# Performance work log

Hardware: AMD Instinct MI355X
Metric: run time of the kernel (lower is better)

## Reference

```python
import jax, jax.numpy as jnp
import numpy as np

N, K, H, W = 2048, 8, 128, 128
G = 50              # glimpse size (50x50 from tem_rnn input 50*50)
ENC = 100           # glimpse encoder output (relation_rnn input arithmetic)
HID = 256
D_REL = ENC + (3 + 50) * 2 + HID          # 462
D_TEM = G * G + (3 + 50) * 2 + HID        # 2862


def _lin(k, out_d, in_d, scale=0.02):
    k1, k2 = jax.random.split(k)
    return (jax.random.normal(k1, (out_d, in_d), jnp.float32) * scale,
            jax.random.normal(k2, (out_d,), jnp.float32) * scale)


def _lstm_params(k, in_d, hid):
    k1, k2, k3, k4 = jax.random.split(k, 4)
    s = 0.02
    return (jax.random.normal(k1, (4 * hid, in_d), jnp.float32) * s,
            jax.random.normal(k2, (4 * hid, hid), jnp.float32) * s,
            jax.random.normal(k3, (4 * hid,), jnp.float32) * s,
            jax.random.normal(k4, (4 * hid,), jnp.float32) * s)


def lstm_cell(x, h, c, Wih, Whh, bih, bhh):
    g = x @ Wih.T + h @ Whh.T + (bih + bhh)
    i, f, gg, o = jnp.split(g, 4, axis=-1)
    i, f, o = jax.nn.sigmoid(i), jax.nn.sigmoid(f), jax.nn.sigmoid(o)
    c2 = f * c + i * jnp.tanh(gg)
    return o * jnp.tanh(c2), c2


def _bilinear_one(im, py, px):
    # im [H,W]; py,px [G,G] pixel coords; zeros padding like torch grid_sample
    x0 = jnp.floor(px); y0 = jnp.floor(py)
    wx1 = px - x0; wy1 = py - y0
    x0i = x0.astype(jnp.int32); y0i = y0.astype(jnp.int32)

    def gather(yi, xi):
        valid = (yi >= 0) & (yi < H) & (xi >= 0) & (xi < W)
        v = im[jnp.clip(yi, 0, H - 1), jnp.clip(xi, 0, W - 1)]
        return jnp.where(valid, v, 0.0)

    return ((1 - wy1) * (1 - wx1) * gather(y0i, x0i)
            + (1 - wy1) * wx1 * gather(y0i, x0i + 1)
            + wy1 * (1 - wx1) * gather(y0i + 1, x0i)
            + wy1 * wx1 * gather(y0i + 1, x0i + 1))


def stn_glimpse(z_where, img):
    # z_where [n,3] = (scale, tx, ty); theta = [[s,0,tx],[0,s,ty]] (attentive_stn_encode)
    s, tx, ty = z_where[:, 0], z_where[:, 1], z_where[:, 2]
    lin = jnp.linspace(-1.0, 1.0, G)
    gy, gx = jnp.meshgrid(lin, lin, indexing='ij')           # [G,G]
    px = (s[:, None, None] * gx + tx[:, None, None] + 1.0) * 0.5 * (W - 1)
    py = (s[:, None, None] * gy + ty[:, None, None] + 1.0) * 0.5 * (H - 1)
    out = jax.vmap(_bilinear_one)(img, py, px)               # [n,G,G]
    return out.reshape(out.shape[0], G * G)


def setup_inputs() -> dict:
    key = jax.random.key(0)
    ks = jax.random.split(key, 16)
    inp = {
        'img': jax.random.uniform(ks[0], (N, H, W), jnp.float32),
        'z_what_last': jax.random.normal(ks[1], (N, K, 50), jnp.float32),
        'z_where_last': jax.random.normal(ks[2], (N, K, 3), jnp.float32) * 0.3,
        'z_pres_last': jnp.ones((N, K, 1), jnp.float32),
        'hidden_last': jax.random.normal(ks[3], (N, K, HID), jnp.float32),
    }
    inp['W_loca'], inp['b_loca'] = _lin(ks[4], 3, HID)
    inp['Wg'], inp['bg'] = _lin(ks[5], ENC, G * G)
    (inp['Wih_rel'], inp['Whh_rel'], inp['bih_rel'], inp['bhh_rel']) = _lstm_params(ks[6], D_REL, HID)
    (inp['Wih_tem'], inp['Whh_tem'], inp['bih_tem'], inp['bhh_tem']) = _lstm_params(ks[7], D_TEM, HID)
    inp['Wm_wh'], inp['bm_wh'] = _lin(ks[8], 3, HID + 3)
    inp['Ws_wh'], inp['bs_wh'] = _lin(ks[9], 3, HID + 3)
    inp['Wm_wt'], inp['bm_wt'] = _lin(ks[10], 50, 50 + HID + HID)
    inp['Ws_wt'], inp['bs_wt'] = _lin(ks[11], 50, 50 + HID + HID)
    inp['Wm_pr'], inp['bm_pr'] = _lin(ks[12], 1, 50 + 3 + HID + HID)
    inp['Ws_pr'], inp['bs_pr'] = _lin(ks[13], 1, 50 + 3 + HID + HID)
    return inp


def reference(img, z_what_last, z_where_last, z_pres_last, hidden_last,
              W_loca, b_loca, Wg, bg,
              Wih_rel, Whh_rel, bih_rel, bhh_rel,
              Wih_tem, Whh_tem, bih_tem, bhh_tem,
              Wm_wh, bm_wh, Ws_wh, bs_wh,
              Wm_wt, bm_wt, Ws_wt, bs_wt,
              Wm_pr, bm_pr, Ws_pr, bs_pr):
    n = img.shape[0]

    def step(carry, xs):
        h_r, c_r, pzw, pzwhat = carry
        zwl, zwhatl, zpl, hl = xs   # [n,3],[n,50],[n,1],[n,256]
        # prop_loca: relu(linear(hidden)) + z_where_last
        zwb = jax.nn.relu(hl @ W_loca.T + b_loca) + zwl
        # STN glimpse + encode (bias pass)
        enc = jax.nn.relu(stn_glimpse(zwb, img) @ Wg.T + bg)        # [n,100]
        rin = jnp.concatenate([enc, zwl, pzw, zwhatl, pzwhat, hl], -1)  # [n,462]
        h_r2, c_r2 = lstm_cell(rin, h_r, c_r, Wih_rel, Whh_rel, bih_rel, bhh_rel)
        # z_where: latent predictor mean (eval mode)
        zw = jnp.concatenate([zwl, h_r2], -1) @ Wm_wh.T + bm_wh      # [n,3]
        # second STN glimpse with sampled where
        g2 = stn_glimpse(zw, img)                                    # [n,2500]
        tin = jnp.concatenate([g2, zw, pzw, zwhatl, pzwhat, hl], -1) # [n,2862]
        h_t, c_t = lstm_cell(tin, h_r2, c_r2, Wih_tem, Whh_tem, bih_tem, bhh_tem)
        # z_what mean
        zwhat = jnp.concatenate([zwhatl, h_r2, h_t], -1) @ Wm_wt.T + bm_wt  # [n,50]
        # z_pres: deterministic expectation of Bernoulli(mean*std) * previous pres
        zp_cal = jnp.concatenate([zwhat, zw, h_r2, h_t], -1)
        p = jax.nn.sigmoid(zp_cal @ Wm_pr.T + bm_pr) * jax.nn.sigmoid(zp_cal @ Ws_pr.T + bs_pr)
        zp = p * zpl                                                 # [n,1]
        return (h_r2, c_r2, zw, zwhat), (zwhat, zw, zp, h_t)

    carry0 = (jnp.zeros((n, HID), img.dtype), jnp.zeros((n, HID), img.dtype),
              jnp.zeros((n, 3), img.dtype), jnp.zeros((n, 50), img.dtype))
    xs = (jnp.swapaxes(z_where_last, 0, 1), jnp.swapaxes(z_what_last, 0, 1),
          jnp.swapaxes(z_pres_last, 0, 1), jnp.swapaxes(hidden_last, 0, 1))
    _, (zwhat_s, zw_s, zp_s, ht_s) = jax.lax.scan(step, carry0, xs)
    z_what = jnp.swapaxes(zwhat_s, 0, 1)   # [n,K,50]
    z_where = jnp.swapaxes(zw_s, 0, 1)     # [n,K,3]
    z_pres = jnp.swapaxes(zp_s, 0, 1)      # [n,K,1]
    h_temp = jnp.swapaxes(ht_s, 0, 1)      # [n,K,256]
    return z_what, z_where, z_pres, h_temp
```

## Files before the change

### kernel.cpp

```cpp
#include <hip/hip_runtime.h>
#include <hip/hip_bf16.h>
#include <math.h>

typedef __attribute__((ext_vector_type(8))) short bf16x8;
typedef __attribute__((ext_vector_type(4))) float f32x4;
using bf16 = __hip_bfloat16;

constexpr int NN   = 2048;
constexpr int KO   = 8;
constexpr int IH   = 128, IW = 128;
constexpr int GS   = 50;
constexpr int HIDD = 256;
constexpr int RIN_LD = 768;
constexpr int TIN_LD = 3136;
constexpr int G1_LD  = 2560;
constexpr int GSTR   = NN*1024;

__device__ __forceinline__ float sigm(float x) { return 1.f/(1.f+expf(-x)); }

template<int OUT_BF16, int RELU>
__global__ __launch_bounds__(256, 4) void mfma_gemm(
    const bf16* __restrict__ A, int lda, int Ktot,
    const bf16* __restrict__ Wt, int ldw, int M,
    const float* __restrict__ b1, const float* __restrict__ b2,
    void* __restrict__ Cout, int ldc, int nxb, int Kseg, int sstride)
{
    __shared__ __align__(16) bf16 As[2*4096];
    __shared__ __align__(16) bf16 Bs[2*4096];
    const int b    = blockIdx.x;
    const int xcd  = b & 7;
    const int t    = b >> 3;
    const int n0   = (xcd + 8*(t / nxb))*64;
    const int m0   = (t % nxb)*64;
    const int tid  = threadIdx.x;
    const int w    = tid>>6, lane = tid&63;
    const int wy   = w>>1, wx = w&1;
    const int q    = lane>>4, fr = lane&15;

    const int kbeg = blockIdx.y * Kseg;
    const int kend = min(Ktot, kbeg + Kseg);
    const int nk   = (kend - kbeg) >> 6;

    const int r0   = tid>>3;
    const int csrc = ((tid&7)*8) ^ ((r0&7)<<3);
    const bf16* pa = A + (size_t)(n0 + r0)*lda + kbeg + csrc;
    int wmr0 = m0 + r0;       if (wmr0 > M-1) wmr0 = M-1;
    int wmr1 = m0 + r0 + 32;  if (wmr1 > M-1) wmr1 = M-1;
    const bf16* pb  = Wt + (size_t)wmr0*ldw + kbeg + csrc;
    const bf16* pb1 = Wt + (size_t)wmr1*ldw + kbeg + csrc;

    f32x4 acc[2][2] = {};

    auto stage = [&](int buf, int koff) {
        bf16* la = As + buf*4096 + w*512;
        bf16* lb = Bs + buf*4096 + w*512;
        __builtin_amdgcn_global_load_lds(
            (const __attribute__((address_space(1))) void*)(pa + koff),
            (__attribute__((address_space(3))) void*)la, 16, 0, 0);
        __builtin_amdgcn_global_load_lds(
            (const __attribute__((address_space(1))) void*)(pa + koff + 32*(size_t)lda),
            (__attribute__((address_space(3))) void*)(la + 2048), 16, 0, 0);
        __builtin_amdgcn_global_load_lds(
            (const __attribute__((address_space(1))) void*)(pb + koff),
            (__attribute__((address_space(3))) void*)lb, 16, 0, 0);
        __builtin_amdgcn_global_load_lds(
            (const __attribute__((address_space(1))) void*)(pb1 + koff),
            (__attribute__((address_space(3))) void*)(lb + 2048), 16, 0, 0);
    };

    stage(0, 0);
    __syncthreads();
    int cur = 0;
    for (int kt = 0; kt < nk; ++kt) {
        if (kt + 1 < nk) stage(cur ^ 1, (kt + 1) << 6);
        const bf16* Ab = As + cur*4096;
        const bf16* Bb = Bs + cur*4096;
        bf16x8 av[2][2], bv[2][2];
        #pragma unroll
        for (int i=0;i<2;i++) {
            int r = wy*32 + i*16 + fr;
            int sw = (r&7)<<3, base = r*64;
            av[i][0] = *(const bf16x8*)(Ab + base + ((q*8) ^ sw));
            av[i][1] = *(const bf16x8*)(Ab + base + ((32 + q*8) ^ sw));
        }
        #pragma unroll
        for (int j=0;j<2;j++) {
            int r = wx*32 + j*16 + fr;
            int sw = (r&7)<<3, base = r*64;
            bv[j][0] = *(const bf16x8*)(Bb + base + ((q*8) ^ sw));
            bv[j][1] = *(const bf16x8*)(Bb + base + ((32 + q*8) ^ sw));
        }
        #pragma unroll
        for (int h=0;h<2;h++)
            #pragma unroll
            for (int i=0;i<2;i++)
                #pragma unroll
                for (int j=0;j<2;j++)
                    acc[i][j] = __builtin_amdgcn_mfma_f32_16x16x32_bf16(av[i][h], bv[j][h], acc[i][j], 0, 0, 0);
        __syncthreads();
        cur ^= 1;
    }

    #pragma unroll
    for (int j=0;j<2;j++) {
        int col = m0 + wx*32 + j*16 + fr;
        if (col < M) {
            float bias = 0.f;
            if (blockIdx.y == 0) {
                if (b1) bias += b1[col];
                if (b2) bias += b2[col];
            }
            #pragma unroll
            for (int i=0;i<2;i++) {
                #pragma unroll
                for (int reg=0;reg<4;reg++) {
                    float v = acc[i][j][reg] + bias;
                    if (RELU) v = fmaxf(v, 0.f);
                    size_t idx = (size_t)(n0 + wy*32 + i*16 + q*4 + reg)*ldc + col;
                    if (OUT_BF16) ((bf16*)Cout)[idx] = __float2bfloat16(v);
                    else          ((float*)Cout)[(size_t)blockIdx.y*sstride + idx] = v;
                }
            }
        }
    }
}

template<int JT>
__global__ __launch_bounds__(256, 2) void gemm128(
    const bf16* __restrict__ A, int lda, int Ktot,
    const bf16* __restrict__ Wt, int ldw,
    const float* __restrict__ b1, const float* __restrict__ b2,
    float* __restrict__ Cout, int ldc, int nxb, int Kseg, int sstride)
{
    constexpr int BMC = JT*32;
    __shared__ __align__(16) bf16 As[128*64];
    __shared__ __align__(16) bf16 Bs[BMC*64];
    const int b    = blockIdx.x;
    const int xcd  = b & 7;
    const int t    = b >> 3;
    const int n0   = (xcd + 8*(t / nxb))*128;
    const int m0   = (t % nxb)*BMC;
    const int tid  = threadIdx.x;
    const int w    = tid>>6, lane = tid&63;
    const int wy   = w>>1, wx = w&1;
    const int q    = lane>>4, fr = lane&15;

    const int kbeg = blockIdx.y * Kseg;
    const int kend = min(Ktot, kbeg + Kseg);
    const int nk   = (kend - kbeg) >> 6;

    const int r0 = tid>>3;
    const int c0 = (tid&7)*8;

    f32x4 acc[4][JT] = {};

    for (int kt = 0; kt < nk; ++kt) {
        const int koff = kbeg + (kt<<6);
        __syncthreads();
        #pragma unroll
        for (int p=0;p<4;p++) {
            int row = p*32 + r0;
            int csrc = c0 ^ ((row&7)<<3);
            __builtin_amdgcn_global_load_lds(
                (const __attribute__((address_space(1))) void*)(A + (size_t)(n0+row)*lda + koff + csrc),
                (__attribute__((address_space(3))) void*)(As + p*2048 + w*512), 16, 0, 0);
        }
        #pragma unroll
        for (int p=0;p<JT;p++) {
            int row = p*32 + r0;
            int csrc = c0 ^ ((row&7)<<3);
            __builtin_amdgcn_global_load_lds(
                (const __attribute__((address_space(1))) void*)(Wt + (size_t)(m0+row)*ldw + koff + csrc),
                (__attribute__((address_space(3))) void*)(Bs + p*2048 + w*512), 16, 0, 0);
        }
        __syncthreads();
        #pragma unroll
        for (int h=0;h<2;h++) {
            bf16x8 av[4], bv[JT];
            #pragma unroll
            for (int i=0;i<4;i++) {
                int r = wy*64 + i*16 + fr;
                av[i] = *(const bf16x8*)(As + r*64 + ((h*32 + q*8) ^ ((r&7)<<3)));
            }
            #pragma unroll
            for (int j=0;j<JT;j++) {
                int r = wx*(JT*16) + j*16 + fr;
                bv[j] = *(const bf16x8*)(Bs + r*64 + ((h*32 + q*8) ^ ((r&7)<<3)));
            }
            #pragma unroll
            for (int i=0;i<4;i++)
                #pragma unroll
                for (int j=0;j<JT;j++)
                    acc[i][j] = __builtin_amdgcn_mfma_f32_16x16x32_bf16(av[i], bv[j], acc[i][j], 0, 0, 0);
        }
    }

    float* Cb = Cout + (size_t)blockIdx.y*sstride;
    #pragma unroll
    for (int j=0;j<JT;j++) {
        int col = m0 + wx*(JT*16) + j*16 + fr;
        float bias = 0.f;
        if (blockIdx.y == 0) {
            if (b1) bias += b1[col];
            if (b2) bias += b2[col];
        }
        #pragma unroll
        for (int i=0;i<4;i++)
            #pragma unroll
            for (int reg=0;reg<4;reg++)
                Cb[(size_t)(n0 + wy*64 + i*16 + q*4 + reg)*ldc + col] = acc[i][j][reg] + bias;
    }
}

__global__ __launch_bounds__(512) void glimpse_all(const float* __restrict__ img,
                                                   const float* __restrict__ zwb,
                                                   bf16* __restrict__ dst, int ldd,
                                                   bf16* __restrict__ rin,
                                                   const float* __restrict__ z_where_last,
                                                   const float* __restrict__ z_what_last,
                                                   const float* __restrict__ hidden_last,
                                                   int cbase, int CH) {
    __shared__ float im_s[IH*IW];
    __shared__ float xw0[KO*50], xw1[KO*50];
    __shared__ int   xi0[KO*50], xi1[KO*50];
    __shared__ float yw0[KO*50], yw1[KO*50];
    __shared__ int   yr0[KO*50], yr1[KO*50];
    const int n = blockIdx.x;
    const float* im = img + (size_t)n*IH*IW;
    {
        const float4* s4 = (const float4*)im;
        float4* d4 = (float4*)im_s;
        for (int t = threadIdx.x; t < IH*IW/4; t += 512) d4[t] = s4[t];
    }
    const float GXS = 2.0f/49.0f;
    for (int t = threadIdx.x; t < CH*100; t += 512) {
        int sl = t / 100, r = t - sl*100;
        const float* zr = zwb + (size_t)(sl*NN + n)*3;
        float s = zr[0];
        if (r < 50) {
            float txp = zr[1] + 1.0f;
            float gx = fmaf((float)r, GXS, -1.0f);
            float px = fmaf(s, gx, txp)*63.5f;
            float x0f = floorf(px); float fa = px - x0f; int x0 = (int)x0f;
            xw0[sl*50+r] = ((unsigned)x0     < 128u) ? (1.f - fa) : 0.f;
            xw1[sl*50+r] = ((unsigned)(x0+1) < 128u) ? fa         : 0.f;
            xi0[sl*50+r] = min(max(x0,  0),127);
            xi1[sl*50+r] = min(max(x0+1,0),127);
        } else {
            int i = r - 50;
            float typ = zr[2] + 1.0f;
            float gy = fmaf((float)i, GXS, -1.0f);
            float py = fmaf(s, gy, typ)*63.5f;
            float y0f = floorf(py); float fy = py - y0f; int y0 = (int)y0f;
            yw0[sl*50+i] = ((unsigned)y0     < 128u) ? (1.f - fy) : 0.f;
            yw1[sl*50+i] = ((unsigned)(y0+1) < 128u) ? fy         : 0.f;
            yr0[sl*50+i] = min(max(y0,  0),127)*IW;
            yr1[sl*50+i] = min(max(y0+1,0),127)*IW;
        }
    }
    __syncthreads();

    const int tot = CH*1250;
    for (int p = threadIdx.x; p < tot; p += 512) {
        int sl = p / 1250, p2 = p - sl*1250;
        int i = p2 / 25, j = (p2 - i*25)*2;
        const float* r0 = im_s + yr0[sl*50+i];
        const float* r1 = im_s + yr1[sl*50+i];
        float wy0 = yw0[sl*50+i], wy1 = yw1[sl*50+i];
        int   a0 = xi0[sl*50+j],     a1 = xi1[sl*50+j];
        float wa0 = xw0[sl*50+j],    wa1 = xw1[sl*50+j];
        int   e0 = xi0[sl*50+j+1],   e1 = xi1[sl*50+j+1];
        float wb0 = xw0[sl*50+j+1],  wb1 = xw1[sl*50+j+1];
        float va = fmaf(wy1, fmaf(wa0, r1[a0], wa1*r1[a1]),
                   wy0 *     fmaf(wa0, r0[a0], wa1*r0[a1]));
        float vb = fmaf(wy1, fmaf(wb0, r1[e0], wb1*r1[e1]),
                   wy0 *     fmaf(wb0, r0[e0], wb1*r0[e1]));
        bf16 b0 = __float2bfloat16(va), b1 = __float2bfloat16(vb);
        unsigned short u0, u1;
        __builtin_memcpy(&u0, &b0, 2); __builtin_memcpy(&u1, &b1, 2);
        bf16* drow = dst + (size_t)(sl*NN + n)*ldd;
        *(unsigned int*)(drow + i*GS + j) = (unsigned)u0 | ((unsigned)u1 << 16);
    }

    const int tot2 = CH*309;
    for (int t = threadIdx.x; t < tot2; t += 512) {
        int sl = t / 309, c = t - sl*309;
        int k = cbase + sl;
        bf16* rrow = rin + (size_t)(sl*NN + n)*RIN_LD;
        float v; int col;
        if (c < 3)       { col = 100 + c;      v = z_where_last[((size_t)n*KO + k)*3 + c]; }
        else if (c < 53) { col = 106 + (c-3);  v = z_what_last[((size_t)n*KO + k)*50 + (c-3)]; }
        else             { col = 206 + (c-53); v = hidden_last[((size_t)n*KO + k)*HIDD + (c-53)]; }
        rrow[col] = __float2bfloat16(v);
    }
}

__global__ __launch_bounds__(256) void rel_glimpse2(
    const float* __restrict__ gates, int nsplit,
    float* __restrict__ h_r, float* __restrict__ c_r,
    const float* __restrict__ z_where_last,
    const float* __restrict__ Wm_wh, const float* __restrict__ bm_wh,
    float* __restrict__ zw_cur, float* __restrict__ out_zwhere,
    bf16* __restrict__ rin_next, bf16* __restrict__ tin,
    const float* __restrict__ img,
    const float* __restrict__ zw_prev, const float* __restrict__ zwhat_prev,
    const float* __restrict__ z_what_last, const float* __restrict__ hidden_last, int k)
{
    __shared__ float hs[256];
    __shared__ float zws[3];
    __shared__ float xw0[50], xw1[50], yw0[50], yw1[50];
    __shared__ int   xi0[50], xi1[50], yr0[50], yr1[50];
    int n = blockIdx.x, j = threadIdx.x;
    float sI=0.f, sF=0.f, sG=0.f, sO=0.f;
    for (int p = 0; p < nsplit; ++p) {
        const float* g = gates + (size_t)p*GSTR + (size_t)n*1024;
        sI += g[j]; sF += g[256+j]; sG += g[512+j]; sO += g[768+j];
    }
    float ig = sigm(sI), fg = sigm(sF), gg = tanhf(sG), og = sigm(sO);
    int cidx = n*256 + j;
    float c2 = fg*c_r[cidx] + ig*gg;
    float hv = og*tanhf(c2);
    c_r[cidx] = c2;
    h_r[cidx] = hv;
    hs[j] = hv;
    bf16 hb = __float2bfloat16(hv);
    rin_next[(size_t)n*RIN_LD + 462 + j] = hb;
    bf16* trow = tin + (size_t)n*TIN_LD;
    trow[2862 + j] = hb;
    __syncthreads();
    int w = j >> 6, lane = j & 63;
    if (w < 3) {
        const float* wt = Wm_wh + w*259;
        float sa = 0.f;
        for (int i = lane; i < 256; i += 64) sa = fmaf(hs[i], wt[3+i], sa);
        #pragma unroll
        for (int off = 32; off; off >>= 1) sa += __shfl_down(sa, off);
        if (lane == 0) {
            const float* zwl = z_where_last + ((size_t)n*KO + k)*3;
            float acc = bm_wh[w] + sa;
            for (int i = 0; i < 3; i++) acc = fmaf(zwl[i], wt[i], acc);
            zws[w] = acc;
            zw_cur[n*3+w] = acc;
            out_zwhere[((size_t)n*KO + k)*3 + w] = acc;
            bf16 ab = __float2bfloat16(acc);
            rin_next[(size_t)n*RIN_LD + 103 + w] = ab;
            trow[2500 + w] = ab;
        }
    }
    __syncthreads();
    {
        const float GXS = 2.0f/49.0f;
        float s = zws[0];
        if (j < 50) {
            float txp = zws[1] + 1.0f;
            float gx = fmaf((float)j, GXS, -1.0f);
            float px = fmaf(s, gx, txp)*63.5f;
            float x0f = floorf(px); float fa = px - x0f; int x0 = (int)x0f;
            xw0[j] = ((unsigned)x0     < 128u) ? (1.f - fa) : 0.f;
            xw1[j] = ((unsigned)(x0+1) < 128u) ? fa         : 0.f;
            xi0[j] = min(max(x0,  0),127);
            xi1[j] = min(max(x0+1,0),127);
        } else if (j < 100) {
            int i = j - 50;
            float typ = zws[2] + 1.0f;
            float gy = fmaf((float)i, GXS, -1.0f);
            float py = fmaf(s, gy, typ)*63.5f;
            float y0f = floorf(py); float fy = py - y0f; int y0 = (int)y0f;
            yw0[i] = ((unsigned)y0     < 128u) ? (1.f - fy) : 0.f;
            yw1[i] = ((unsigned)(y0+1) < 128u) ? fy         : 0.f;
            yr0[i] = min(max(y0,  0),127)*IW;
            yr1[i] = min(max(y0+1,0),127)*IW;
        }
    }
    __syncthreads();
    const float* im = img + (size_t)n*IH*IW;
    for (int p2 = j; p2 < 1250; p2 += 256) {
        int i = p2 / 25, jj = (p2 - i*25)*2;
        const float* r0 = im + yr0[i];
        const float* r1 = im + yr1[i];
        float wy0 = yw0[i], wy1 = yw1[i];
        int   a0 = xi0[jj],    a1 = xi1[jj];
        float wa0 = xw0[jj],   wa1 = xw1[jj];
        int   e0 = xi0[jj+1],  e1 = xi1[jj+1];
        float wb0 = xw0[jj+1], wb1 = xw1[jj+1];
        float va = fmaf(wy1, fmaf(wa0, r1[a0], wa1*r1[a1]),
                   wy0 *     fmaf(wa0, r0[a0], wa1*r0[a1]));
        float vb = fmaf(wy1, fmaf(wb0, r1[e0], wb1*r1[e1]),
                   wy0 *     fmaf(wb0, r0[e0], wb1*r0[e1]));
        bf16 b0 = __float2bfloat16(va), b1 = __float2bfloat16(vb);
        unsigned short u0, u1;
        __builtin_memcpy(&u0, &b0, 2); __builtin_memcpy(&u1, &b1, 2);
        *(unsigned int*)(trow + i*GS + jj) = (unsigned)u0 | ((unsigned)u1 << 16);
    }
    for (int c = 3 + j; c < 362; c += 256) {
        float v;
        if      (c <   6) v = zw_prev[n*3 + c-3];
        else if (c <  56) v = z_what_last[((size_t)n*KO + k)*50 + c-6];
        else if (c < 106) v = zwhat_prev[n*50 + c-56];
        else              v = hidden_last[((size_t)n*KO + k)*HIDD + c-106];
        trow[2500 + c] = __float2bfloat16(v);
    }
}

__global__ void zero_f32(float* __restrict__ p, int n) {
    int i = blockIdx.x*blockDim.x + threadIdx.x;
    if (i < n) p[i] = 0.f;
}

__global__ void repack_w(const float* __restrict__ s1, int K1,
                         const float* __restrict__ s2, int K2,
                         bf16* __restrict__ dst, int ldd, int M) {
    int gid = blockIdx.x*blockDim.x + threadIdx.x;
    if (gid >= M*ldd) return;
    int m = gid / ldd, c = gid - m*ldd;
    float v = 0.f;
    if (c < K1)           v = s1[(size_t)m*K1 + c];
    else if (c < K1+K2)   v = s2[(size_t)m*K2 + (c-K1)];
    dst[gid] = __float2bfloat16(v);
}

__global__ void transpose_wmwt(const float* __restrict__ W, float* __restrict__ Wt) {
    int gid = blockIdx.x*blockDim.x + threadIdx.x;
    if (gid >= 576*64) return;
    int i = gid >> 6, m = gid & 63;
    Wt[gid] = (m < 50 && i < 562) ? W[(size_t)m*562 + i] : 0.f;
}

__global__ __launch_bounds__(256) void zwb_all_v2(const float* __restrict__ hidden_last,
                                                  const float* __restrict__ z_where_last,
                                                  const float* __restrict__ Wl, const float* __restrict__ bl,
                                                  float* __restrict__ zwb_all) {
    __shared__ float wls[768];
    for (int i = threadIdx.x; i < 768; i += 256) wls[i] = Wl[i];
    __syncthreads();
    int wv = threadIdx.x>>6, lane = threadIdx.x&63;
    int row = blockIdx.x*4 + wv;
    int s = row >> 11, n = row & (NN-1);
    const float* hl = hidden_last + ((size_t)n*KO + s)*HIDD;
    float4 h4 = *(const float4*)(hl + lane*4);
    float s0=0.f, s1=0.f, s2=0.f;
    #pragma unroll
    for (int r4=0;r4<4;r4++) {
        float hv = ((const float*)&h4)[r4];
        int i = lane*4 + r4;
        s0 = fmaf(hv, wls[i],     s0);
        s1 = fmaf(hv, wls[256+i], s1);
        s2 = fmaf(hv, wls[512+i], s2);
    }
    #pragma unroll
    for (int off=32; off; off>>=1) {
        s0 += __shfl_down(s0,off); s1 += __shfl_down(s1,off); s2 += __shfl_down(s2,off);
    }
    if (lane == 0) {
        const float* zwl = z_where_last + ((size_t)n*KO + s)*3;
        zwb_all[row*3+0] = fmaxf(s0+bl[0],0.f) + zwl[0];
        zwb_all[row*3+1] = fmaxf(s1+bl[1],0.f) + zwl[1];
        zwb_all[row*3+2] = fmaxf(s2+bl[2],0.f) + zwl[2];
    }
}

__global__ void zero_rin_carry(bf16* __restrict__ rin0) {
    int gid = blockIdx.x*blockDim.x + threadIdx.x;
    if (gid >= NN*309) return;
    int c = gid % 309, n = gid/309;
    int col = (c < 3) ? 103+c : ((c < 53) ? 156+(c-3) : 462+(c-53));
    rin0[(size_t)n*RIN_LD + col] = __float2bfloat16(0.f);
}

__global__ __launch_bounds__(256) void tem_fused(
    const float* __restrict__ gates, int nsplit,
    const float* __restrict__ c_r, const float* __restrict__ h_r,
    const float* __restrict__ z_what_last,
    const float* __restrict__ wt_t, const float* __restrict__ bm_wt,
    const float* __restrict__ Wm_pr, const float* __restrict__ bm_pr,
    const float* __restrict__ Ws_pr, const float* __restrict__ bs_pr,
    const float* __restrict__ zw_cur, const float* __restrict__ z_pres_last,
    float* __restrict__ zwhat_cur, float* __restrict__ out_zwhat,
    float* __restrict__ out_htemp, float* __restrict__ out_zpres,
    bf16* __restrict__ rin_next, int k)
{
    __shared__ float L[615];
    __shared__ float part[4][64];
    int n = blockIdx.x, j = threadIdx.x;
    float sI=0.f, sF=0.f, sG=0.f, sO=0.f;
    for (int p = 0; p < nsplit; ++p) {
        const float* g = gates + (size_t)p*GSTR + (size_t)n*1024;
        sI += g[j]; sF += g[256+j]; sG += g[512+j]; sO += g[768+j];
    }
    float ig = sigm(sI), fg = sigm(sF), gg = tanhf(sG), og = sigm(sO);
    float c2 = fg*c_r[n*256+j] + ig*gg;
    float hv = og*tanhf(c2);
    out_htemp[((size_t)n*KO + k)*HIDD + j] = hv;
    L[309+j] = hv;
    L[53+j]  = h_r[n*256+j];
    if (j < 50)      L[j]  = z_what_last[((size_t)n*KO + k)*50 + j];
    else if (j < 53) L[j]  = zw_cur[n*3 + (j-50)];
    __syncthreads();
    {
        int m = j & 63, grp = j >> 6;
        float sa = 0.f;
        for (int i = grp; i < 562; i += 4) {
            float v = (i < 50) ? L[i] : L[i+3];
            sa = fmaf(v, wt_t[i*64 + m], sa);
        }
        part[grp][m] = sa;
    }
    __syncthreads();
    if (j < 50) {
        float acc = part[0][j] + part[1][j] + part[2][j] + part[3][j] + bm_wt[j];
        zwhat_cur[n*50+j] = acc;
        out_zwhat[((size_t)n*KO + k)*50 + j] = acc;
        rin_next[(size_t)n*RIN_LD + 156 + j] = __float2bfloat16(acc);
        L[565+j] = acc;
    }
    __syncthreads();
    if (j < 64) {
        float s1 = 0.f, s2 = 0.f;
        for (int i = j; i < 565; i += 64) {
            float v = (i < 50) ? L[565+i] : L[i];
            s1 = fmaf(v, Wm_pr[i], s1);
            s2 = fmaf(v, Ws_pr[i], s2);
        }
        #pragma unroll
        for (int off = 32; off; off >>= 1) { s1 += __shfl_down(s1,off); s2 += __shfl_down(s2,off); }
        if (j == 0) {
            float p = sigm(s1 + bm_pr[0]) * sigm(s2 + bs_pr[0]);
            out_zpres[(size_t)n*KO + k] = p * z_pres_last[(size_t)n*KO + k];
        }
    }
}

extern "C" void kernel_launch(void* const* d_in, const int* in_sizes, int n_in,
                              void* d_out, int out_size, void* d_ws, size_t ws_size,
                              hipStream_t stream) {
    (void)in_sizes; (void)n_in; (void)out_size;
    const float* img          = (const float*)d_in[0];
    const float* z_what_last  = (const float*)d_in[1];
    const float* z_where_last = (const float*)d_in[2];
    const float* z_pres_last  = (const float*)d_in[3];
    const float* hidden_last  = (const float*)d_in[4];
    const float* W_loca = (const float*)d_in[5];
    const float* b_loca = (const float*)d_in[6];
    const float* Wg     = (const float*)d_in[7];
    const float* bg     = (const float*)d_in[8];
    const float* Wih_rel = (const float*)d_in[9];
    const float* Whh_rel = (const float*)d_in[10];
    const float* bih_rel = (const float*)d_in[11];
    const float* bhh_rel = (const float*)d_in[12];
    const float* Wih_tem = (const float*)d_in[13];
    const float* Whh_tem = (const float*)d_in[14];
    const float* bih_tem = (const float*)d_in[15];
    const float* bhh_tem = (const float*)d_in[16];
    const float* Wm_wh = (const float*)d_in[17];
    const float* bm_wh = (const float*)d_in[18];
    const float* Wm_wt = (const float*)d_in[21];
    const float* bm_wt = (const float*)d_in[22];
    const float* Wm_pr = (const float*)d_in[25];
    const float* bm_pr = (const float*)d_in[26];
    const float* Ws_pr = (const float*)d_in[27];
    const float* bs_pr = (const float*)d_in[28];

    char* base_p = (char*)d_ws;
    size_t off = 0;
    auto carve = [&](size_t bytes) -> char* {
        char* r = base_p + off;
        off += (bytes + 255) & ~(size_t)255;
        return r;
    };
    bf16*  tin      = (bf16*) carve((size_t)NN*TIN_LD*2);
    float* gates    = (float*)carve((size_t)4*NN*1024*4);
    bf16*  W_tem    = (bf16*) carve((size_t)1024*TIN_LD*2);
    bf16*  W_rel    = (bf16*) carve((size_t)1024*RIN_LD*2);
    bf16*  Wg_bf    = (bf16*) carve((size_t)100*G1_LD*2);
    float* wt_t     = (float*)carve((size_t)576*64*4);
    float* zwb_all  = (float*)carve((size_t)KO*NN*3*4);
    float* h_r      = (float*)carve((size_t)NN*HIDD*4);
    float* c_r      = (float*)carve((size_t)NN*HIDD*4);
    float* zw1      = (float*)carve((size_t)NN*3*4);
    float* zwhat1   = (float*)carve((size_t)NN*50*4);
    float* zw0      = (float*)carve((size_t)NN*3*4);
    float* zwhat0   = (float*)carve((size_t)NN*50*4);
    size_t fixed_bytes = off;

    int CH = 1;
    for (int cand : {8, 4, 2}) {
        size_t need = fixed_bytes
                    + (((size_t)cand*NN*G1_LD*2 + 255) & ~(size_t)255)
                    + (((size_t)cand*NN*RIN_LD*2 + 255) & ~(size_t)255);
        if (need <= ws_size) { CH = cand; break; }
    }
    bf16* g1 = nullptr; int g1ld;
    bf16* rin;
    if (CH > 1) {
        g1   = (bf16*)carve((size_t)CH*NN*G1_LD*2);
        rin  = (bf16*)carve((size_t)CH*NN*RIN_LD*2);
        g1ld = G1_LD;
    } else {
        rin  = (bf16*)carve((size_t)NN*RIN_LD*2);
        g1   = tin;
        g1ld = TIN_LD;
    }

    float* out        = (float*)d_out;
    float* out_zwhat  = out;
    float* out_zwhere = out + (size_t)NN*KO*50;
    float* out_zpres  = out_zwhere + (size_t)NN*KO*3;
    float* out_htemp  = out_zpres + (size_t)NN*KO;

    {
        int nz = NN*(HIDD + 3 + 50);
        zero_f32<<<(nz+255)/256, 256, 0, stream>>>(c_r, nz);
    }
    zero_rin_carry<<<(NN*309+255)/256, 256, 0, stream>>>(rin);
    repack_w<<<((1024*RIN_LD)+255)/256, 256, 0, stream>>>(Wih_rel, 462, Whh_rel, 256, W_rel, RIN_LD, 1024);
    repack_w<<<((1024*TIN_LD)+255)/256, 256, 0, stream>>>(Wih_tem, 2862, Whh_tem, 256, W_tem, TIN_LD, 1024);
    repack_w<<<((100*G1_LD)+255)/256, 256, 0, stream>>>(Wg, 2500, nullptr, 0, Wg_bf, G1_LD, 100);
    transpose_wmwt<<<(576*64+255)/256, 256, 0, stream>>>(Wm_wt, wt_t);
    zwb_all_v2<<<KO*NN/4, 256, 0, stream>>>(hidden_last, z_where_last, W_loca, b_loca, zwb_all);

    for (int cbase = 0; cbase < KO; cbase += CH) {
        glimpse_all<<<NN, 512, 0, stream>>>(img, zwb_all + (size_t)cbase*NN*3, g1, g1ld,
                                            rin, z_where_last, z_what_last, hidden_last, cbase, CH);
        mfma_gemm<1,1><<<dim3(2*CH*32,1), 256, 0, stream>>>(g1, g1ld, G1_LD, Wg_bf, G1_LD, 100,
                                                            bg, nullptr, rin, RIN_LD, 2, G1_LD, 0);

        for (int s = 0; s < CH; ++s) {
            int k = cbase + s;
            bf16* rin_k  = rin + (size_t)s*NN*RIN_LD;
            bf16* rin_nx = rin + (size_t)((s+1)%CH)*NN*RIN_LD;
            float* zw_cur     = (k & 1) ? zw1 : zw0;
            float* zw_prev    = (k & 1) ? zw0 : zw1;
            float* zwhat_cur  = (k & 1) ? zwhat1 : zwhat0;
            float* zwhat_prev = (k & 1) ? zwhat0 : zwhat1;

            gemm128<2><<<dim3(256,2), 256, 0, stream>>>(rin_k, RIN_LD, RIN_LD, W_rel, RIN_LD,
                                                        bih_rel, bhh_rel, gates, 1024, 16, 384, GSTR);
            rel_glimpse2<<<NN, 256, 0, stream>>>(gates, 2, h_r, c_r, z_where_last, Wm_wh, bm_wh,
                                                 zw_cur, out_zwhere, rin_nx, tin,
                                                 img, zw_prev, zwhat_prev, z_what_last, hidden_last, k);
            gemm128<4><<<dim3(128,4), 256, 0, stream>>>(tin, TIN_LD, TIN_LD, W_tem, TIN_LD,
                                                        bih_tem, bhh_tem, gates, 1024, 8, 832, GSTR);
            tem_fused<<<NN, 256, 0, stream>>>(gates, 4, c_r, h_r, z_what_last, wt_t, bm_wt, Wm_pr, bm_pr, Ws_pr, bs_pr,
                                              zw_cur, z_pres_last, zwhat_cur, out_zwhat, out_htemp, out_zpres, rin_nx, k);
        }
    }
}
```

Before: 1.126 ms.

## Fuse glimpse sampling with encoder GEMM and reshape temporal GEMM split

The glimpse kernel now samples straight from global memory, with no LDS copy of the image. It keeps the bf16 glimpse tile for all objects in LDS and runs the 100-output encoder matmul with MFMA inside the same block, writing ReLU outputs into the relation input. This removes the separate glimpse buffer, its global round trip and the extra GEMM launch. The temporal LSTM GEMM switches from a 4-way to a 2-way K split with narrower tiles, which halves the partial-sum gate storage that tem_fused has to read. Risks are uncoalesced global image gathers, and the in-block MFMA using only 7 waves with strided global weight loads.

```diff
diff --git a/kernel.cpp b/kernel.cpp
--- a/kernel.cpp
+++ b/kernel.cpp
@@ -13,117 +13,10 @@
 constexpr int HIDD = 256;
 constexpr int RIN_LD = 768;
 constexpr int TIN_LD = 3136;
-constexpr int G1_LD  = 2560;
+constexpr int WG_LD  = 2560;
 constexpr int GSTR   = NN*1024;
 
 __device__ __forceinline__ float sigm(float x) { return 1.f/(1.f+expf(-x)); }
-
-template<int OUT_BF16, int RELU>
-__global__ __launch_bounds__(256, 4) void mfma_gemm(
-    const bf16* __restrict__ A, int lda, int Ktot,
-    const bf16* __restrict__ Wt, int ldw, int M,
-    const float* __restrict__ b1, const float* __restrict__ b2,
-    void* __restrict__ Cout, int ldc, int nxb, int Kseg, int sstride)
-{
-    __shared__ __align__(16) bf16 As[2*4096];
-    __shared__ __align__(16) bf16 Bs[2*4096];
-    const int b    = blockIdx.x;
-    const int xcd  = b & 7;
-    const int t    = b >> 3;
-    const int n0   = (xcd + 8*(t / nxb))*64;
-    const int m0   = (t % nxb)*64;
-    const int tid  = threadIdx.x;
-    const int w    = tid>>6, lane = tid&63;
-    const int wy   = w>>1, wx = w&1;
-    const int q    = lane>>4, fr = lane&15;
-
-    const int kbeg = blockIdx.y * Kseg;
-    const int kend = min(Ktot, kbeg + Kseg);
-    const int nk   = (kend - kbeg) >> 6;
-
-    const int r0   = tid>>3;
-    const int csrc = ((tid&7)*8) ^ ((r0&7)<<3);
-    const bf16* pa = A + (size_t)(n0 + r0)*lda + kbeg + csrc;
-    int wmr0 = m0 + r0;       if (wmr0 > M-1) wmr0 = M-1;
-    int wmr1 = m0 + r0 + 32;  if (wmr1 > M-1) wmr1 = M-1;
-    const bf16* pb  = Wt + (size_t)wmr0*ldw + kbeg + csrc;
-    const bf16* pb1 = Wt + (size_t)wmr1*ldw + kbeg + csrc;
-
-    f32x4 acc[2][2] = {};
-
-    auto stage = [&](int buf, int koff) {
-        bf16* la = As + buf*4096 + w*512;
-        bf16* lb = Bs + buf*4096 + w*512;
-        __builtin_amdgcn_global_load_lds(
-            (const __attribute__((address_space(1))) void*)(pa + koff),
-            (__attribute__((address_space(3))) void*)la, 16, 0, 0);
-        __builtin_amdgcn_global_load_lds(
-            (const __attribute__((address_space(1))) void*)(pa + koff + 32*(size_t)lda),
-            (__attribute__((address_space(3))) void*)(la + 2048), 16, 0, 0);
-        __builtin_amdgcn_global_load_lds(
-            (const __attribute__((address_space(1))) void*)(pb + koff),
-            (__attribute__((address_space(3))) void*)lb, 16, 0, 0);
-        __builtin_amdgcn_global_load_lds(
-            (const __attribute__((address_space(1))) void*)(pb1 + koff),
-            (__attribute__((address_space(3))) void*)(lb + 2048), 16, 0, 0);
-    };
-
-    stage(0, 0);
-    __syncthreads();
-    int cur = 0;
-    for (int kt = 0; kt < nk; ++kt) {
-        if (kt + 1 < nk) stage(cur ^ 1, (kt + 1) << 6);
-        const bf16* Ab = As + cur*4096;
-        const bf16* Bb = Bs + cur*4096;
-        bf16x8 av[2][2], bv[2][2];
-        #pragma unroll
-        for (int i=0;i<2;i++) {
-            int r = wy*32 + i*16 + fr;
-            int sw = (r&7)<<3, base = r*64;
-            av[i][0] = *(const bf16x8*)(Ab + base + ((q*8) ^ sw));
-            av[i][1] = *(const bf16x8*)(Ab + base + ((32 + q*8) ^ sw));
-        }
-        #pragma unroll
-        for (int j=0;j<2;j++) {
-            int r = wx*32 + j*16 + fr;
-            int sw = (r&7)<<3, base = r*64;
-            bv[j][0] = *(const bf16x8*)(Bb + base + ((q*8) ^ sw));
-            bv[j][1] = *(const bf16x8*)(Bb + base + ((32 + q*8) ^ sw));
-        }
-        #pragma unroll
-        for (int h=0;h<2;h++)
-            #pragma unroll
-            for (int i=0;i<2;i++)
-                #pragma unroll
-                for (int j=0;j<2;j++)
-                    acc[i][j] = __builtin_amdgcn_mfma_f32_16x16x32_bf16(av[i][h], bv[j][h], acc[i][j], 0, 0, 0);
-        __syncthreads();
-        cur ^= 1;
-    }
-
-    #pragma unroll
-    for (int j=0;j<2;j++) {
-        int col = m0 + wx*32 + j*16 + fr;
-        if (col < M) {
-            float bias = 0.f;
-            if (blockIdx.y == 0) {
-                if (b1) bias += b1[col];
-                if (b2) bias += b2[col];
-            }
-            #pragma unroll
-            for (int i=0;i<2;i++) {
-                #pragma unroll
-                for (int reg=0;reg<4;reg++) {
-                    float v = acc[i][j][reg] + bias;
-                    if (RELU) v = fmaxf(v, 0.f);
-                    size_t idx = (size_t)(n0 + wy*32 + i*16 + q*4 + reg)*ldc + col;
-                    if (OUT_BF16) ((bf16*)Cout)[idx] = __float2bfloat16(v);
-                    else          ((float*)Cout)[(size_t)blockIdx.y*sstride + idx] = v;
-                }
-            }
-        }
-    }
-}
 
 template<int JT>
 __global__ __launch_bounds__(256, 2) void gemm128(
@@ -212,28 +105,25 @@
     }
 }
 
-__global__ __launch_bounds__(512) void glimpse_all(const float* __restrict__ img,
-                                                   const float* __restrict__ zwb,
-                                                   bf16* __restrict__ dst, int ldd,
-                                                   bf16* __restrict__ rin,
-                                                   const float* __restrict__ z_where_last,
-                                                   const float* __restrict__ z_what_last,
-                                                   const float* __restrict__ hidden_last,
-                                                   int cbase, int CH) {
-    __shared__ float im_s[IH*IW];
-    __shared__ float xw0[KO*50], xw1[KO*50];
-    __shared__ int   xi0[KO*50], xi1[KO*50];
-    __shared__ float yw0[KO*50], yw1[KO*50];
-    __shared__ int   yr0[KO*50], yr1[KO*50];
-    const int n = blockIdx.x;
-    const float* im = img + (size_t)n*IH*IW;
-    {
-        const float4* s4 = (const float4*)im;
-        float4* d4 = (float4*)im_s;
-        for (int t = threadIdx.x; t < IH*IW/4; t += 512) d4[t] = s4[t];
-    }
+__global__ __launch_bounds__(512) void glimpse_enc(
+    const float* __restrict__ img,
+    const float* __restrict__ zwb,
+    const bf16*  __restrict__ Wg_bf,
+    const float* __restrict__ bg,
+    bf16* __restrict__ rin,
+    const float* __restrict__ z_where_last,
+    const float* __restrict__ z_what_last,
+    const float* __restrict__ hidden_last,
+    int cbase, int CH)
+{
+    __shared__ float xw0[8*50], xw1[8*50], yw0[8*50], yw1[8*50];
+    __shared__ int   xi01[8*50], yro01[8*50];
+    __shared__ __align__(16) unsigned g_u[8*1264];
+    const int n   = blockIdx.x;
+    const int tid = threadIdx.x;
     const float GXS = 2.0f/49.0f;
-    for (int t = threadIdx.x; t < CH*100; t += 512) {
+
+    for (int t = tid; t < CH*100; t += 512) {
         int sl = t / 100, r = t - sl*100;
         const float* zr = zwb + (size_t)(sl*NN + n)*3;
         float s = zr[0];
@@ -244,8 +134,7 @@
             float x0f = floorf(px); float fa = px - x0f; int x0 = (int)x0f;
             xw0[sl*50+r] = ((unsigned)x0     < 128u) ? (1.f - fa) : 0.f;
             xw1[sl*50+r] = ((unsigned)(x0+1) < 128u) ? fa         : 0.f;
-            xi0[sl*50+r] = min(max(x0,  0),127);
-            xi1[sl*50+r] = min(max(x0+1,0),127);
+            xi01[sl*50+r] = min(max(x0,0),127) | (min(max(x0+1,0),127) << 16);
         } else {
             int i = r - 50;
             float typ = zr[2] + 1.0f;
@@ -254,23 +143,29 @@
             float y0f = floorf(py); float fy = py - y0f; int y0 = (int)y0f;
             yw0[sl*50+i] = ((unsigned)y0     < 128u) ? (1.f - fy) : 0.f;
             yw1[sl*50+i] = ((unsigned)(y0+1) < 128u) ? fy         : 0.f;
-            yr0[sl*50+i] = min(max(y0,  0),127)*IW;
-            yr1[sl*50+i] = min(max(y0+1,0),127)*IW;
-        }
-    }
-    __syncthreads();
-
+            yro01[sl*50+i] = (min(max(y0,0),127)*IW) | ((min(max(y0+1,0),127)*IW) << 16);
+        }
+    }
+    for (int t = tid; t < 8*14; t += 512) {
+        int sl = t / 14;
+        g_u[sl*1264 + 1250 + (t - sl*14)] = 0u;
+    }
+    __syncthreads();
+
+    const float* im = img + (size_t)n*IH*IW;
     const int tot = CH*1250;
-    for (int p = threadIdx.x; p < tot; p += 512) {
+    for (int p = tid; p < tot; p += 512) {
         int sl = p / 1250, p2 = p - sl*1250;
-        int i = p2 / 25, j = (p2 - i*25)*2;
-        const float* r0 = im_s + yr0[sl*50+i];
-        const float* r1 = im_s + yr1[sl*50+i];
+        int i = p2 / 25, jh = p2 - i*25;
+        int j = jh*2;
+        int yy = yro01[sl*50+i];
+        const float* r0 = im + (yy & 0xffff);
+        const float* r1 = im + (yy >> 16);
         float wy0 = yw0[sl*50+i], wy1 = yw1[sl*50+i];
-        int   a0 = xi0[sl*50+j],     a1 = xi1[sl*50+j];
-        float wa0 = xw0[sl*50+j],    wa1 = xw1[sl*50+j];
-        int   e0 = xi0[sl*50+j+1],   e1 = xi1[sl*50+j+1];
-        float wb0 = xw0[sl*50+j+1],  wb1 = xw1[sl*50+j+1];
+        int xa = xi01[sl*50+j];   int a0 = xa & 0xffff, a1 = xa >> 16;
+        float wa0 = xw0[sl*50+j], wa1 = xw1[sl*50+j];
+        int xb = xi01[sl*50+j+1]; int e0 = xb & 0xffff, e1 = xb >> 16;
+        float wb0 = xw0[sl*50+j+1], wb1 = xw1[sl*50+j+1];
         float va = fmaf(wy1, fmaf(wa0, r1[a0], wa1*r1[a1]),
                    wy0 *     fmaf(wa0, r0[a0], wa1*r0[a1]));
         float vb = fmaf(wy1, fmaf(wb0, r1[e0], wb1*r1[e1]),
@@ -278,12 +173,10 @@
         bf16 b0 = __float2bfloat16(va), b1 = __float2bfloat16(vb);
         unsigned short u0, u1;
         __builtin_memcpy(&u0, &b0, 2); __builtin_memcpy(&u1, &b1, 2);
-        bf16* drow = dst + (size_t)(sl*NN + n)*ldd;
-        *(unsigned int*)(drow + i*GS + j) = (unsigned)u0 | ((unsigned)u1 << 16);
-    }
-
-    const int tot2 = CH*309;
-    for (int t = threadIdx.x; t < tot2; t += 512) {
+        g_u[sl*1264 + i*25 + jh] = (unsigned)u0 | ((unsigned)u1 << 16);
+    }
+
+    for (int t = tid; t < CH*309; t += 512) {
         int sl = t / 309, c = t - sl*309;
         int k = cbase + sl;
         bf16* rrow = rin + (size_t)(sl*NN + n)*RIN_LD;
@@ -292,6 +185,32 @@
         else if (c < 53) { col = 106 + (c-3);  v = z_what_last[((size_t)n*KO + k)*50 + (c-3)]; }
         else             { col = 206 + (c-53); v = hidden_last[((size_t)n*KO + k)*HIDD + (c-53)]; }
         rrow[col] = __float2bfloat16(v);
+    }
+    __syncthreads();
+
+    int w = tid>>6, lane = tid&63;
+    if (w < 7) {
+        const unsigned* ga = g_u + (lane&7)*1264 + (lane>>4)*4;
+        const bf16* wbp = Wg_bf + (size_t)(w*16 + (lane&15))*WG_LD + (lane>>4)*8;
+        f32x4 acc = {};
+        for (int kk = 0; kk < 79; ++kk) {
+            bf16x8 a = *(const bf16x8*)(ga + kk*16);
+            bf16x8 bb = *(const bf16x8*)(wbp + kk*32);
+            acc = __builtin_amdgcn_mfma_f32_16x16x32_bf16(a, bb, acc, 0, 0, 0);
+        }
+        int col = w*16 + (lane&15);
+        int q = lane>>4;
+        if (col < 100 && q < 2) {
+            float bias = bg[col];
+            #pragma unroll
+            for (int reg = 0; reg < 4; ++reg) {
+                int sl = q*4 + reg;
+                if (sl < CH) {
+                    float v = fmaxf(acc[reg] + bias, 0.f);
+                    rin[(size_t)(sl*NN + n)*RIN_LD + col] = __float2bfloat16(v);
+                }
+            }
+        }
     }
 }
 
@@ -409,13 +328,15 @@
 
 __global__ void repack_w(const float* __restrict__ s1, int K1,
                          const float* __restrict__ s2, int K2,
-                         bf16* __restrict__ dst, int ldd, int M) {
+                         bf16* __restrict__ dst, int ldd, int M, int Mv) {
     int gid = blockIdx.x*blockDim.x + threadIdx.x;
     if (gid >= M*ldd) return;
     int m = gid / ldd, c = gid - m*ldd;
     float v = 0.f;
-    if (c < K1)           v = s1[(size_t)m*K1 + c];
-    else if (c < K1+K2)   v = s2[(size_t)m*K2 + (c-K1)];
+    if (m < Mv) {
+        if (c < K1)           v = s1[(size_t)m*K1 + c];
+        else if (c < K1+K2)   v = s2[(size_t)m*K2 + (c-K1)];
+    }
     dst[gid] = __float2bfloat16(v);
 }
 
@@ -568,10 +489,10 @@
         return r;
     };
     bf16*  tin      = (bf16*) carve((size_t)NN*TIN_LD*2);
-    float* gates    = (float*)carve((size_t)4*NN*1024*4);
+    float* gates    = (float*)carve((size_t)2*NN*1024*4);
     bf16*  W_tem    = (bf16*) carve((size_t)1024*TIN_LD*2);
     bf16*  W_rel    = (bf16*) carve((size_t)1024*RIN_LD*2);
-    bf16*  Wg_bf    = (bf16*) carve((size_t)100*G1_LD*2);
+    bf16*  Wg_bf    = (bf16*) carve((size_t)112*WG_LD*2);
     float* wt_t     = (float*)carve((size_t)576*64*4);
     float* zwb_all  = (float*)carve((size_t)KO*NN*3*4);
     float* h_r      = (float*)carve((size_t)NN*HIDD*4);
@@ -584,22 +505,10 @@
 
     int CH = 1;
     for (int cand : {8, 4, 2}) {
-        size_t need = fixed_bytes
-                    + (((size_t)cand*NN*G1_LD*2 + 255) & ~(size_t)255)
-                    + (((size_t)cand*NN*RIN_LD*2 + 255) & ~(size_t)255);
+        size_t need = fixed_bytes + (((size_t)cand*NN*RIN_LD*2 + 255) & ~(size_t)255);
         if (need <= ws_size) { CH = cand; break; }
     }
-    bf16* g1 = nullptr; int g1ld;
-    bf16* rin;
-    if (CH > 1) {
-        g1   = (bf16*)carve((size_t)CH*NN*G1_LD*2);
-        rin  = (bf16*)carve((size_t)CH*NN*RIN_LD*2);
-        g1ld = G1_LD;
-    } else {
-        rin  = (bf16*)carve((size_t)NN*RIN_LD*2);
-        g1   = tin;
-        g1ld = TIN_LD;
-    }
+    bf16* rin = (bf16*)carve((size_t)CH*NN*RIN_LD*2);
 
     float* out        = (float*)d_out;
     float* out_zwhat  = out;
@@ -612,17 +521,15 @@
         zero_f32<<<(nz+255)/256, 256, 0, stream>>>(c_r, nz);
     }
     zero_rin_carry<<<(NN*309+255)/256, 256, 0, stream>>>(rin);
-    repack_w<<<((1024*RIN_LD)+255)/256, 256, 0, stream>>>(Wih_rel, 462, Whh_rel, 256, W_rel, RIN_LD, 1024);
-    repack_w<<<((1024*TIN_LD)+255)/256, 256, 0, stream>>>(Wih_tem, 2862, Whh_tem, 256, W_tem, TIN_LD, 1024);
-    repack_w<<<((100*G1_LD)+255)/256, 256, 0, stream>>>(Wg, 2500, nullptr, 0, Wg_bf, G1_LD, 100);
+    repack_w<<<((1024*RIN_LD)+255)/256, 256, 0, stream>>>(Wih_rel, 462, Whh_rel, 256, W_rel, RIN_LD, 1024, 1024);
+    repack_w<<<((1024*TIN_LD)+255)/256, 256, 0, stream>>>(Wih_tem, 2862, Whh_tem, 256, W_tem, TIN_LD, 1024, 1024);
+    repack_w<<<((112*WG_LD)+255)/256, 256, 0, stream>>>(Wg, 2500, nullptr, 0, Wg_bf, WG_LD, 112, 100);
     transpose_wmwt<<<(576*64+255)/256, 256, 0, stream>>>(Wm_wt, wt_t);
     zwb_all_v2<<<KO*NN/4, 256, 0, stream>>>(hidden_last, z_where_last, W_loca, b_loca, zwb_all);
 
     for (int cbase = 0; cbase < KO; cbase += CH) {
-        glimpse_all<<<NN, 512, 0, stream>>>(img, zwb_all + (size_t)cbase*NN*3, g1, g1ld,
+        glimpse_enc<<<NN, 512, 0, stream>>>(img, zwb_all + (size_t)cbase*NN*3, Wg_bf, bg,
                                             rin, z_where_last, z_what_last, hidden_last, cbase, CH);
-        mfma_gemm<1,1><<<dim3(2*CH*32,1), 256, 0, stream>>>(g1, g1ld, G1_LD, Wg_bf, G1_LD, 100,
-                                                            bg, nullptr, rin, RIN_LD, 2, G1_LD, 0);
 
         for (int s = 0; s < CH; ++s) {
             int k = cbase + s;
@@ -638,9 +545,9 @@
             rel_glimpse2<<<NN, 256, 0, stream>>>(gates, 2, h_r, c_r, z_where_last, Wm_wh, bm_wh,
                                                  zw_cur, out_zwhere, rin_nx, tin,
                                                  img, zw_prev, zwhat_prev, z_what_last, hidden_last, k);
-            gemm128<4><<<dim3(128,4), 256, 0, stream>>>(tin, TIN_LD, TIN_LD, W_tem, TIN_LD,
-                                                        bih_tem, bhh_tem, gates, 1024, 8, 832, GSTR);
-            tem_fused<<<NN, 256, 0, stream>>>(gates, 4, c_r, h_r, z_what_last, wt_t, bm_wt, Wm_pr, bm_pr, Ws_pr, bs_pr,
+            gemm128<2><<<dim3(256,2), 256, 0, stream>>>(tin, TIN_LD, TIN_LD, W_tem, TIN_LD,
+                                                        bih_tem, bhh_tem, gates, 1024, 16, 1600, GSTR);
+            tem_fused<<<NN, 256, 0, stream>>>(gates, 2, c_r, h_r, z_what_last, wt_t, bm_wt, Wm_pr, bm_pr, Ws_pr, bs_pr,
                                               zw_cur, z_pres_last, zwhat_cur, out_zwhat, out_htemp, out_zpres, rin_nx, k);
         }
     }
```

Result: slower. 1.224 ms (+8.8%).
